# Performance work log

Hardware: AMD Instinct MI355X
Metric: run time of the kernel (lower is better)

The kernel has to match this reference:

```python
import jax, jax.numpy as jnp
import numpy as np

N, E = 16384, 262144
NS_N, NV_N = 128, 64      # node irreps: 128x0e + 64x1o
NS_E, NV_E = 64, 32       # edge irreps: 64x0e + 32x1o
C_OH, LAT = 16, 128
DS, DV = 128, 64          # irreps_out: 128x0e + 64x1o
GS = DS + DV              # gate input scalars (128 act scalars + 64 gates)
SC = 2 * NS_N + NS_E      # 320 concatenated scalar channels
VC = 2 * NV_N + NV_E      # 160 concatenated l=1 channels
M0_IN = SC + VC           # 480 m=0 features into SO2 linear
M0_OUT = GS + DV          # 256 m=0 outputs
AVG_NEI = 16.0
EPS = 1e-8


def setup_inputs() -> dict:
    key = jax.random.key(0)
    ks = jax.random.split(key, 20)
    f = lambda k, s: jax.random.normal(k, s, dtype=jnp.float32)
    return dict(
        node_feat=f(ks[0], (N, NS_N + 3 * NV_N)),
        edge_feat=f(ks[1], (E, NS_E + 3 * NV_E)),
        edge_vec=f(ks[2], (E, 3)),
        latents=f(ks[3], (E, LAT)),
        node_onehot=jax.nn.one_hot(jax.random.randint(ks[4], (N,), 0, C_OH), C_OH, dtype=jnp.float32),
        ln_n_g0=jnp.ones(NS_N), ln_n_b0=jnp.zeros(NS_N), ln_n_g1=jnp.ones(NV_N),
        ln_e_g0=jnp.ones(NS_E), ln_e_b0=jnp.zeros(NS_E), ln_e_g1=jnp.ones(NV_E),
        W_m0=f(ks[5], (M0_IN, M0_OUT)),
        w_r=f(ks[6], (VC, DV)), w_i=f(ks[7], (VC, DV)),
        W_env=f(ks[8], (LAT, DS + DV)),
        Wp0=f(ks[9], (DS, DS)), bp0=jnp.zeros(DS), Wpv=f(ks[10], (DV, DV)),
        Wtp0=f(ks[11], (DS, C_OH, GS)), Wtp1=f(ks[12], (DV, C_OH, DV)),
        Wo0=f(ks[13], (DS, DS)), bo0=jnp.zeros(DS), Wov=f(ks[14], (DV, DV)),
        res_param=jnp.zeros(()),
        edge_index=jax.random.randint(ks[15], (2, E), 0, N),
    )


def _sep_ln(s, v, g0, b0, g1):
    # separable equivariant layer norm: LN on scalars, per-sample RMS on l=1 block
    mu = s.mean(-1, keepdims=True)
    var = jnp.mean((s - mu) ** 2, -1, keepdims=True)
    s = (s - mu) * jax.lax.rsqrt(var + EPS) * g0 + b0
    vvar = jnp.mean(v * v, axis=(-2, -1), keepdims=True)  # component norm, degree-balanced (single l=1)
    v = v * jax.lax.rsqrt(vvar + EPS) * g1[None, :, None]
    return s, v


def _edge_frame(vec):
    # orthonormal frame (a, e1, e2) with a along the edge
    a = vec * jax.lax.rsqrt(jnp.sum(vec * vec, -1, keepdims=True) + EPS)
    helper = jnp.where(jnp.abs(a[:, 2:3]) < 0.99,
                       jnp.array([0.0, 0.0, 1.0], dtype=vec.dtype),
                       jnp.array([1.0, 0.0, 0.0], dtype=vec.dtype))
    e1 = jnp.cross(helper, a)
    e1 = e1 * jax.lax.rsqrt(jnp.sum(e1 * e1, -1, keepdims=True) + EPS)
    e2 = jnp.cross(a, e1)
    return a, e1, e2


def reference(node_feat, edge_feat, edge_vec, latents, node_onehot,
              ln_n_g0, ln_n_b0, ln_n_g1, ln_e_g0, ln_e_b0, ln_e_g1,
              W_m0, w_r, w_i, W_env, Wp0, bp0, Wpv,
              Wtp0, Wtp1, Wo0, bo0, Wov, res_param, edge_index):
    src, dst = edge_index[0], edge_index[1]
    ns, nv = node_feat[:, :NS_N], node_feat[:, NS_N:].reshape(-1, NV_N, 3)
    es, ev = edge_feat[:, :NS_E], edge_feat[:, NS_E:].reshape(-1, NV_E, 3)
    ns, nv = _sep_ln(ns, nv, ln_n_g0, ln_n_b0, ln_n_g1)
    es, ev = _sep_ln(es, ev, ln_e_g0, ln_e_b0, ln_e_g1)
    # per-edge concat: node[src] + edge + node[dst]
    s_cat = jnp.concatenate([ns[src], es, ns[dst]], -1)          # [E, SC]
    v_cat = jnp.concatenate([nv[src], ev, nv[dst]], 1)           # [E, VC, 3]
    # SO2 linear: rotate into edge frame, mix per |m|, rotate back
    a, e1, e2 = _edge_frame(edge_vec)
    c0 = jnp.einsum('eci,ei->ec', v_cat, a)
    c1 = jnp.einsum('eci,ei->ec', v_cat, e1)
    c2 = jnp.einsum('eci,ei->ec', v_cat, e2)
    m0 = jnp.concatenate([s_cat, c0], -1) @ W_m0 * (1.0 / np.sqrt(M0_IN))  # [E, M0_OUT]
    s_out, c0o = m0[:, :GS], m0[:, GS:]
    inv = 1.0 / np.sqrt(VC)
    c1o = (c1 @ w_r - c2 @ w_i) * inv
    c2o = (c1 @ w_i + c2 @ w_r) * inv
    v_out = (c0o[..., None] * a[:, None, :] + c1o[..., None] * e1[:, None, :]
             + c2o[..., None] * e2[:, None, :])                  # [E, DV, 3]
    # gate activation
    s_act = jax.nn.silu(s_out[:, :DS])
    gates = jax.nn.sigmoid(s_out[:, DS:])
    v_g = v_out * gates[..., None]
    # lin_post (per-l linear, scalar bias)
    s2 = s_act @ Wp0 * (1.0 / np.sqrt(DS)) + bp0
    v2 = jnp.einsum('eui,uv->evi', v_g, Wpv) * (1.0 / np.sqrt(DV))
    # env weighting from latents (E3ElementLinear, per-irrep-channel scalars)
    w = latents @ W_env * (1.0 / np.sqrt(LAT))
    s2 = s2 * w[:, :DS]
    v2 = v2 * w[:, DS:, None]
    nrm = 1.0 / np.sqrt(AVG_NEI)
    sa = jax.ops.segment_sum(s2, dst, num_segments=N) * nrm
    va = jax.ops.segment_sum(v2, dst, num_segments=N) * nrm
    # one-hot FullyConnectedTensorProduct (in2 all 0e) + gate + linear
    t0 = jnp.einsum('nu,nc,ucv->nv', sa, node_onehot, Wtp0) * (1.0 / np.sqrt(DS * C_OH))
    t1 = jnp.einsum('nui,nc,ucv->nvi', va, node_onehot, Wtp1) * (1.0 / np.sqrt(DV * C_OH))
    s3 = jax.nn.silu(t0[:, :DS])
    v3 = t1 * jax.nn.sigmoid(t0[:, DS:])[..., None]
    s4 = s3 @ Wo0 * (1.0 / np.sqrt(DS)) + bo0
    v4 = jnp.einsum('nui,uv->nvi', v3, Wov) * (1.0 / np.sqrt(DV))
    new = jnp.concatenate([s4, v4.reshape(-1, 3 * DV)], -1)
    r = jax.nn.sigmoid(res_param)
    return r * node_feat + (1.0 - r) * new
```

## Files before the change

kernel.cpp:

```cpp
#include <hip/hip_runtime.h>
#include <math.h>

#define N_NODES 16384
#define N_EDGES 262144
#define EPSF 1e-8f

#define OFF_XE    0
#define OFF_C12   14848
#define OFF_FR    35840
#define OFF_EDST  36608
#define OFF_ESRC  36736
#define POOL_BYTES 36864
#define OFF_SACT  0
#define OFF_GATE  8704
#define OFF_C0O   13312
#define OFF_C1O   17920
#define OFF_C2O   22528
#define OFF_VG    8704

typedef __bf16 bf16x8 __attribute__((ext_vector_type(8)));
typedef float  f32x4  __attribute__((ext_vector_type(4)));

__device__ __forceinline__ f32x4 MFMA16(bf16x8 a, bf16x8 b, f32x4 c){
  return __builtin_amdgcn_mfma_f32_16x16x32_bf16(a, b, c, 0, 0, 0);
// ... 87 lines not shown
}

__global__ __launch_bounds__(256) void k_node_ln(
    const float* __restrict__ nf, const float* __restrict__ g0,
    const float* __restrict__ b0, const float* __restrict__ g1,
    unsigned short* __restrict__ ns_ln, _Float16* __restrict__ nv_ln)
{
  const int tid  = threadIdx.x;
  const int lane = tid & 63;
  const int n    = blockIdx.x*4 + (tid>>6);
  const float* row = nf + (size_t)n*320;

  float s0 = row[lane], s1 = row[64+lane];
  float mu = wsum64(s0+s1) * (1.0f/128.0f);
  float d0 = s0-mu, d1 = s1-mu;
  float var = wsum64(d0*d0+d1*d1) * (1.0f/128.0f);
  float rs = rsqrtf(var + EPSF);
  ns_ln[(size_t)n*128 + lane]    = f2bf(d0*rs*g0[lane]    + b0[lane]);
  ns_ln[(size_t)n*128 + 64+lane] = f2bf(d1*rs*g0[64+lane] + b0[64+lane]);

  float px = row[128+lane*3+0], py = row[128+lane*3+1], pz = row[128+lane*3+2];
  float vvar = wsum64(px*px+py*py+pz*pz) * (1.0f/192.0f);
  float vsc = rsqrtf(vvar + EPSF) * g1[lane];
  nv_ln[(size_t)n*192 + lane*3+0] = (_Float16)(px*vsc);
  nv_ln[(size_t)n*192 + lane*3+1] = (_Float16)(py*vsc);
  nv_ln[(size_t)n*192 + lane*3+2] = (_Float16)(pz*vsc);
}

__global__ __launch_bounds__(256,4) void k_edge(
  const float* __restrict__ ef, const float* __restrict__ evec,
  const float* __restrict__ lats,
  const float* __restrict__ g0e, const float* __restrict__ b0e, const float* __restrict__ g1e,
  const unsigned short* __restrict__ pWm0, const unsigned short* __restrict__ pWc,
  const unsigned short* __restrict__ pWenv, const unsigned short* __restrict__ pWp0,
  const unsigned short* __restrict__ pWpv,
  const float* __restrict__ bp0,
  const int* __restrict__ eidx, const int* __restrict__ perm,
  const unsigned short* __restrict__ ns_ln, const _Float16* __restrict__ nv_ln,
  float* __restrict__ sa, float* __restrict__ va)
{
  extern __shared__ unsigned char pool[];
  const int tid = threadIdx.x;
  unsigned short* XE   = (unsigned short*)(pool + OFF_XE);
  unsigned short* C12s = (unsigned short*)(pool + OFF_C12);
  _Float16* FRh = (_Float16*)(pool + OFF_FR);
  int* EDST = (int*)(pool + OFF_EDST);
  int* ESRC = (int*)(pool + OFF_ESRC);

  const int nwg = gridDim.x;
  const int bswz = (blockIdx.x & 7)*(nwg>>3) + (blockIdx.x >> 3);

  const int wid = tid>>6, l = tid&63;
  const int r15 = l&15, g = l>>4;
  const int sbase = bswz*32;

  {
    const int ln = tid & 31;
    int psrc[4], pdst[4];
    float pvx[4], pvy[4], pvz[4];
    float pef0[4], pef1[4], pwx[4], pwy[4], pwz[4];
    #pragma unroll
    for (int eo=0; eo<4; ++eo){
      const int slot = sbase + eo*8 + (tid>>5);
      const int e = perm[slot];
      psrc[eo] = eidx[e];
      pdst[eo] = eidx[N_EDGES + e];
      pvx[eo] = evec[(size_t)e*3+0];
      pvy[eo] = evec[(size_t)e*3+1];
      pvz[eo] = evec[(size_t)e*3+2];
      const float* erow = ef + (size_t)e*160;
      pef0[eo] = erow[ln];
      pef1[eo] = erow[32+ln];
      pwx[eo]  = erow[64+ln*3+0];
      pwy[eo]  = erow[64+ln*3+1];
      pwz[eo]  = erow[64+ln*3+2];
    }
    _Float16 pns[4][6], pnd[4][6];
    #pragma unroll
    for (int eo=0; eo<4; ++eo){
      const _Float16* nvs = nv_ln + (size_t)psrc[eo]*192 + 3*ln;
      const _Float16* nvd = nv_ln + (size_t)pdst[eo]*192 + 3*ln;
      pns[eo][0]=nvs[0];  pns[eo][1]=nvs[1];  pns[eo][2]=nvs[2];
      pns[eo][3]=nvs[96]; pns[eo][4]=nvs[97]; pns[eo][5]=nvs[98];
      pnd[eo][0]=nvd[0];  pnd[eo][1]=nvd[1];  pnd[eo][2]=nvd[2];
      pnd[eo][3]=nvd[96]; pnd[eo][4]=nvd[97]; pnd[eo][5]=nvd[98];
    }

    #pragma unroll
    for (int eo=0; eo<4; ++eo){
      const int el = eo*8 + (tid>>5);
      const int src = psrc[eo];
      const int dst = pdst[eo];

      float vx=pvx[eo], vy=pvy[eo], vz=pvz[eo];
      float rn = rsqrtf(vx*vx+vy*vy+vz*vz+EPSF);
      float ax=vx*rn, ay=vy*rn, az=vz*rn;
      float hx, hz;
      if (fabsf(az) < 0.99f){ hx=0.f; hz=1.f; } else { hx=1.f; hz=0.f; }
      float e1x = -hz*ay;
      float e1y = hz*ax - hx*az;
      float e1z = hx*ay;
      float rn1 = rsqrtf(e1x*e1x+e1y*e1y+e1z*e1z+EPSF);
      e1x*=rn1; e1y*=rn1; e1z*=rn1;
      float e2x = ay*e1z - az*e1y;
      float e2y = az*e1x - ax*e1z;
      float e2z = ax*e1y - ay*e1x;
      if (ln==0){
        FRh[el*12+0]=(_Float16)ax;  FRh[el*12+1]=(_Float16)ay;  FRh[el*12+2]=(_Float16)az;
        FRh[el*12+3]=(_Float16)e1x; FRh[el*12+4]=(_Float16)e1y; FRh[el*12+5]=(_Float16)e1z;
        FRh[el*12+6]=(_Float16)e2x; FRh[el*12+7]=(_Float16)e2y; FRh[el*12+8]=(_Float16)e2z;
        EDST[el]=dst;
        ESRC[el]=src;
      }

      float s0=pef0[eo], s1=pef1[eo];
      float mu = wsum32(s0+s1)*(1.f/64.f);
      float d0=s0-mu, d1=s1-mu;
      float var = wsum32(d0*d0+d1*d1)*(1.f/64.f);
      float rs = rsqrtf(var+EPSF);
      XE[el*232 + ln]    = f2bf(d0*rs*g0e[ln]    + b0e[ln]);
      XE[el*232 + 32+ln] = f2bf(d1*rs*g0e[32+ln] + b0e[32+ln]);

      float wx=pwx[eo], wy=pwy[eo], wz=pwz[eo];
      float vvar = wsum32(wx*wx+wy*wy+wz*wz)*(1.f/96.f);
      float vsc = rsqrtf(vvar+EPSF)*g1e[ln];
      wx*=vsc; wy*=vsc; wz*=vsc;
      XE  [el*232 + 64+64+ln]    = f2bf(wx*ax +wy*ay +wz*az);
      C12s[el*328 + 64+ln]       = f2bf(wx*e1x+wy*e1y+wz*e1z);
      C12s[el*328 + 160+64+ln]   = f2bf(wx*e2x+wy*e2y+wz*e2z);

      #pragma unroll
      for (int q=0;q<2;q++){
        int u = ln+32*q;
        float px=(float)pns[eo][q*3+0], py=(float)pns[eo][q*3+1], pz=(float)pns[eo][q*3+2];
        XE  [el*232 + 64+u]      = f2bf(px*ax +py*ay +pz*az);
        C12s[el*328 + u]         = f2bf(px*e1x+py*e1y+pz*e1z);
        C12s[el*328 + 160+u]     = f2bf(px*e2x+py*e2y+pz*e2z);
        px=(float)pnd[eo][q*3+0]; py=(float)pnd[eo][q*3+1]; pz=(float)pnd[eo][q*3+2];
        XE  [el*232 + 64+96+u]   = f2bf(px*ax +py*ay +pz*az);
        C12s[el*328 + 96+u]      = f2bf(px*e1x+py*e1y+pz*e1z);
        C12s[el*328 + 160+96+u]  = f2bf(px*e2x+py*e2y+pz*e2z);
      }
    }
  }
  __syncthreads();

  const f32x4 zero4 = {0.f,0.f,0.f,0.f};

  f32x4 acc1[2][4];
  #pragma unroll
  for (int m=0;m<2;m++)
    #pragma unroll
    for (int n=0;n<4;n++) acc1[m][n]=zero4;
  {
    const unsigned short* bbase = pWm0 + ((size_t)(wid*64 + r15)*4 + g)*8;
    bf16x8 gA[2][8];
    {
      const int rs0 = ESRC[r15], rs1 = ESRC[16+r15];
      const int rd0 = EDST[r15], rd1 = EDST[16+r15];
      #pragma unroll
      for (int q=0;q<4;q++){
        gA[0][q]   = *(const bf16x8*)&ns_ln[(size_t)rs0*128 + q*32 + g*8];
        gA[1][q]   = *(const bf16x8*)&ns_ln[(size_t)rs1*128 + q*32 + g*8];
        gA[0][4+q] = *(const bf16x8*)&ns_ln[(size_t)rd0*128 + q*32 + g*8];
        gA[1][4+q] = *(const bf16x8*)&ns_ln[(size_t)rd1*128 + q*32 + g*8];
      }
    }
    #pragma unroll
    for (int t=0;t<7;t++){
      const int kc  = (t<2) ? (4+t) : (10 + t-2);
      const int col = (t<2) ? (t*32) : (64 + (t-2)*32);
      bf16x8 a0 = *(const bf16x8*)&XE[(    r15)*232 + col + g*8];
      bf16x8 a1 = *(const bf16x8*)&XE[(16+ r15)*232 + col + g*8];
      const unsigned short* bp = bbase + (size_t)kc*8192;
      #pragma unroll
      for (int n=0;n<4;n++){
        bf16x8 b = *(const bf16x8*)(bp + n*512);
        acc1[0][n] = MFMA16(a0,b,acc1[0][n]);
        acc1[1][n] = MFMA16(a1,b,acc1[1][n]);
      }
    }
    #pragma unroll
    for (int t=0;t<8;t++){
      const int kc = (t<4) ? t : (6 + t-4);
      const unsigned short* bp = bbase + (size_t)kc*8192;
      #pragma unroll
      for (int n=0;n<4;n++){
        bf16x8 b = *(const bf16x8*)(bp + n*512);
        acc1[0][n] = MFMA16(gA[0][t],b,acc1[0][n]);
        acc1[1][n] = MFMA16(gA[1][t],b,acc1[1][n]);
      }
    }
  }

  f32x4 acc2[2][2];
  #pragma unroll
  for (int m=0;m<2;m++){ acc2[m][0]=zero4; acc2[m][1]=zero4; }
  {
    const unsigned short* bbase = pWc + ((size_t)(wid*32 + r15)*4 + g)*8;
    #pragma unroll
    for (int kc=0;kc<10;kc++){
      bf16x8 a0 = *(const bf16x8*)&C12s[(    r15)*328 + kc*32 + g*8];
      bf16x8 a1 = *(const bf16x8*)&C12s[(16+ r15)*328 + kc*32 + g*8];
      const unsigned short* bp = bbase + (size_t)kc*4096;
      #pragma unroll
      for (int n=0;n<2;n++){
        bf16x8 b = *(const bf16x8*)(bp + n*512);
        acc2[0][n] = MFMA16(a0,b,acc2[0][n]);
        acc2[1][n] = MFMA16(a1,b,acc2[1][n]);
      }
    }
  }

  float wsc[2][2][4], wvc[2][4];
  {
    f32x4 acc3[2][3];
    #pragma unroll
    for (int m=0;m<2;m++)
      #pragma unroll
      for (int n=0;n<3;n++) acc3[m][n]=zero4;
    const int eg0 = perm[sbase + r15];
    const int eg1 = perm[sbase + 16 + r15];
    const float* la0 = lats + (size_t)eg0*128;
    const float* la1 = lats + (size_t)eg1*128;
    const int colb0 = wid*32, colb1 = wid*32+16, colb2 = 128+wid*16;
    #pragma unroll
    for (int kc=0;kc<4;kc++){
      float4 f00 = *(const float4*)&la0[kc*32 + g*8];
      float4 f01 = *(const float4*)&la0[kc*32 + g*8 + 4];
      float4 f10 = *(const float4*)&la1[kc*32 + g*8];
      float4 f11 = *(const float4*)&la1[kc*32 + g*8 + 4];
      union { bf16x8 v; unsigned short s[8]; } a0, a1;
      a0.s[0]=f2bf(f00.x); a0.s[1]=f2bf(f00.y); a0.s[2]=f2bf(f00.z); a0.s[3]=f2bf(f00.w);
      a0.s[4]=f2bf(f01.x); a0.s[5]=f2bf(f01.y); a0.s[6]=f2bf(f01.z); a0.s[7]=f2bf(f01.w);
      a1.s[0]=f2bf(f10.x); a1.s[1]=f2bf(f10.y); a1.s[2]=f2bf(f10.z); a1.s[3]=f2bf(f10.w);
      a1.s[4]=f2bf(f11.x); a1.s[5]=f2bf(f11.y); a1.s[6]=f2bf(f11.z); a1.s[7]=f2bf(f11.w);
      bf16x8 b0 = *(const bf16x8*)(pWenv + ((size_t)(kc*192 + colb0 + r15)*4 + g)*8);
      bf16x8 b1 = *(const bf16x8*)(pWenv + ((size_t)(kc*192 + colb1 + r15)*4 + g)*8);
      bf16x8 b2 = *(const bf16x8*)(pWenv + ((size_t)(kc*192 + colb2 + r15)*4 + g)*8);
      acc3[0][0] = MFMA16(a0.v,b0,acc3[0][0]);
      acc3[1][0] = MFMA16(a1.v,b0,acc3[1][0]);
      acc3[0][1] = MFMA16(a0.v,b1,acc3[0][1]);
      acc3[1][1] = MFMA16(a1.v,b1,acc3[1][1]);
      acc3[0][2] = MFMA16(a0.v,b2,acc3[0][2]);
      acc3[1][2] = MFMA16(a1.v,b2,acc3[1][2]);
    }
    const float S = 0.08838834764831845f;
    #pragma unroll
    for (int m=0;m<2;m++)
      #pragma unroll
      for (int r=0;r<4;r++){
        wsc[m][0][r] = acc3[m][0][r]*S;
        wsc[m][1][r] = acc3[m][1][r]*S;
        wvc[m][r]    = acc3[m][2][r]*S;
      }
  }

  float bp0v[2];
  #pragma unroll
  for (int n=0;n<2;n++) bp0v[n] = bp0[wid*32 + n*16 + r15];

  __syncthreads();

  {
    unsigned short* SAs = (unsigned short*)(pool + OFF_SACT);
    unsigned short* GAb = (unsigned short*)(pool + OFF_GATE);
    unsigned short* C0b = (unsigned short*)(pool + OFF_C0O);
    #pragma unroll
    for (int m=0;m<2;m++)
      #pragma unroll
      for (int n=0;n<4;n++)
        #pragma unroll
        for (int r=0;r<4;r++){
          int e = m*16 + g*4 + r;
          int j = wid*64 + n*16 + r15;
          float v = acc1[m][n][r]*0.04564354645876384f;
          if (j < 128)      SAs[e*136 + j] = f2bf(silu(v));
          else if (j < 192) GAb[e*72 + (j-128)] = f2bf(sigm(v));
          else              C0b[e*72 + (j-192)] = f2bf(v);
        }
    unsigned short* C1b = (unsigned short*)(pool + OFF_C1O);
    unsigned short* C2b = (unsigned short*)(pool + OFF_C2O);
    #pragma unroll
    for (int m=0;m<2;m++)
      #pragma unroll
      for (int n=0;n<2;n++)
        #pragma unroll
        for (int r=0;r<4;r++){
          int e = m*16 + g*4 + r;
          int j = wid*32 + n*16 + r15;
          float v = acc2[m][n][r]*0.07905694150420949f;
          if (j < 64) C1b[e*72 + j] = f2bf(v);
          else        C2b[e*72 + (j-64)] = f2bf(v);
        }
  }
  __syncthreads();

  {
    const int e = tid>>3, u0 = (tid&7)*8;
    const unsigned short* GAb = (const unsigned short*)(pool + OFF_GATE);
    const unsigned short* C0b = (const unsigned short*)(pool + OFF_C0O);
    const unsigned short* C1b = (const unsigned short*)(pool + OFF_C1O);
    const unsigned short* C2b = (const unsigned short*)(pool + OFF_C2O);
    float ax=(float)FRh[e*12+0],  ay=(float)FRh[e*12+1],  az=(float)FRh[e*12+2];
    float b1x=(float)FRh[e*12+3], b1y=(float)FRh[e*12+4], b1z=(float)FRh[e*12+5];
    float b2x=(float)FRh[e*12+6], b2y=(float)FRh[e*12+7], b2z=(float)FRh[e*12+8];
    float vgx[8], vgy[8], vgz[8];
    #pragma unroll
    for (int i=0;i<8;i++){
      int u = u0+i;
      float gt = bf2f(GAb[e*72+u]);
      float c0 = bf2f(C0b[e*72+u]), c1 = bf2f(C1b[e*72+u]), c2 = bf2f(C2b[e*72+u]);
      vgx[i] = (c0*ax + c1*b1x + c2*b2x)*gt;
      vgy[i] = (c0*ay + c1*b1y + c2*b2y)*gt;
      vgz[i] = (c0*az + c1*b1z + c2*b2z)*gt;
    }
    __syncthreads();
    unsigned short* VGs = (unsigned short*)(pool + OFF_VG);
    #pragma unroll
    for (int i=0;i<8;i++){
      VGs[0*2304 + e*72 + u0+i] = f2bf(vgx[i]);
      VGs[1*2304 + e*72 + u0+i] = f2bf(vgy[i]);
      VGs[2*2304 + e*72 + u0+i] = f2bf(vgz[i]);
    }
  }
  __syncthreads();

  {
    const unsigned short* SAs = (const unsigned short*)(pool + OFF_SACT);
    const unsigned short* VGs = (const unsigned short*)(pool + OFF_VG);

    f32x4 acc4[2][2], acc5[3][2];
    #pragma unroll
    for (int m=0;m<2;m++){ acc4[m][0]=zero4; acc4[m][1]=zero4; }
    #pragma unroll
    for (int c=0;c<3;c++){ acc5[c][0]=zero4; acc5[c][1]=zero4; }

    {
      const unsigned short* bbase = pWp0 + ((size_t)(wid*32 + r15)*4 + g)*8;
      #pragma unroll
      for (int kc=0;kc<4;kc++){
        bf16x8 a0 = *(const bf16x8*)&SAs[(    r15)*136 + kc*32 + g*8];
        bf16x8 a1 = *(const bf16x8*)&SAs[(16+ r15)*136 + kc*32 + g*8];
        #pragma unroll
        for (int n=0;n<2;n++){
          bf16x8 b = *(const bf16x8*)(bbase + (size_t)kc*4096 + n*512);
          acc4[0][n] = MFMA16(a0,b,acc4[0][n]);
          acc4[1][n] = MFMA16(a1,b,acc4[1][n]);
        }
      }
    }
    {
      bf16x8 b5[2];
      #pragma unroll
      for (int kc=0;kc<2;kc++)
        b5[kc] = *(const bf16x8*)(pWpv + ((size_t)(kc*64 + wid*16 + r15)*4 + g)*8);
      #pragma unroll
      for (int c=0;c<3;c++)
        #pragma unroll
        for (int kc=0;kc<2;kc++){
          bf16x8 a0 = *(const bf16x8*)&VGs[c*2304 + (    r15)*72 + kc*32 + g*8];
          bf16x8 a1 = *(const bf16x8*)&VGs[c*2304 + (16+ r15)*72 + kc*32 + g*8];
          acc5[c][0] = MFMA16(a0,b5[kc],acc5[c][0]);
          acc5[c][1] = MFMA16(a1,b5[kc],acc5[c][1]);
        }
    }

    __syncthreads();
    _Float16* R = (_Float16*)pool;
    #pragma unroll
    for (int m=0;m<2;m++)
      #pragma unroll
      for (int n=0;n<2;n++)
        #pragma unroll
        for (int r=0;r<4;r++){
          int e = m*16 + g*4 + r;
          int j = wid*32 + n*16 + r15;
          R[e*320 + j] = (_Float16)((acc4[m][n][r]*0.08838834764831845f + bp0v[n]) * wsc[m][n][r]);
        }
    #pragma unroll
    for (int c=0;c<3;c++)
      #pragma unroll
      for (int m=0;m<2;m++)
        #pragma unroll
        for (int r=0;r<4;r++){
          int e = m*16 + g*4 + r;
          int vch = wid*16 + r15;
          R[e*320 + 128 + vch*3 + c] = (_Float16)(acc5[c][m][r]*0.125f * wvc[m][r]);
        }
    __syncthreads();

    for (int j = tid; j < 320; j += 256){
      float accv = (float)R[j];
      int cur = EDST[0];
      for (int e=1;e<32;e++){
        int d = EDST[e];
        float v = (float)R[e*320 + j];
        if (d != cur){
          float* tgt = (j<128) ? &sa[(size_t)cur*128 + j] : &va[(size_t)cur*192 + (j-128)];
          atomicAdd(tgt, accv);
          accv = v; cur = d;
        } else accv += v;
      }
      float* tgt = (j<128) ? &sa[(size_t)cur*128 + j] : &va[(size_t)cur*192 + (j-128)];
      atomicAdd(tgt, accv);
    }
  }
}

__global__ __launch_bounds__(256) void k_node_out(
  const float* __restrict__ nf, const float* __restrict__ oh,
  const float* __restrict__ Wtp0, const float* __restrict__ Wtp1,
  const float* __restrict__ Wo0, const float* __restrict__ bo0,
  const float* __restrict__ Wov, const float* __restrict__ resp,
  const float* __restrict__ sa, const float* __restrict__ va,
  float* __restrict__ out)
{
  __shared__ float SAB[4][128];
  __shared__ float VX[4][64], VY[4][64], VZ[4][64];
  __shared__ float S3 [4][128];
  __shared__ float V3 [4][256];
  const int tid=threadIdx.x, lane=tid&63, g=tid>>6;
  const int n = blockIdx.x*4 + g;

  float cf=0.f;
  #pragma unroll
  for (int j=0;j<16;j++) cf += j*oh[(size_t)n*16+j];
  const int c = (int)(cf+0.5f);

  SAB[g][lane]    = sa[(size_t)n*128+lane]   *0.25f;
  SAB[g][64+lane] = sa[(size_t)n*128+64+lane]*0.25f;
  VX[g][lane] = va[(size_t)n*192+lane*3+0]*0.25f;
  VY[g][lane] = va[(size_t)n*192+lane*3+1]*0.25f;
  VZ[g][lane] = va[(size_t)n*192+lane*3+2]*0.25f;
  __syncthreads();

  float t00=0.f, t01=0.f, t02=0.f;
  const float* w0c = Wtp0 + (size_t)c*192;
  for (int u=0;u<128;u++){
    float s = SAB[g][u];
    t00 += s * w0c[(size_t)u*3072 + lane];
    t01 += s * w0c[(size_t)u*3072 + lane+64];
    t02 += s * w0c[(size_t)u*3072 + lane+128];
  }
  const float sct0 = 0.02209708691f;
  t00*=sct0; t01*=sct0; t02*=sct0;

  float t1x=0.f,t1y=0.f,t1z=0.f;
  const float* w1c = Wtp1 + (size_t)c*64;
  for (int u=0;u<64;u++){
    float wv = w1c[(size_t)u*1024 + lane];
    t1x += VX[g][u]*wv;
    t1y += VY[g][u]*wv;
    t1z += VZ[g][u]*wv;
  }
  t1x*=0.03125f; t1y*=0.03125f; t1z*=0.03125f;

  S3[g][lane]    = silu(t00);
// ... 37 lines not shown
  const float* nf   = (const float*)d_in[0];
  const float* ef   = (const float*)d_in[1];
  const float* evec = (const float*)d_in[2];
  const float* lats = (const float*)d_in[3];
  const float* oh   = (const float*)d_in[4];
  const float* g0n  = (const float*)d_in[5];
  const float* b0n  = (const float*)d_in[6];
  const float* g1n  = (const float*)d_in[7];
  const float* g0e  = (const float*)d_in[8];
  const float* b0e  = (const float*)d_in[9];
  const float* g1e  = (const float*)d_in[10];
  const float* Wm0  = (const float*)d_in[11];
  const float* wr   = (const float*)d_in[12];
  const float* wi   = (const float*)d_in[13];
  const float* Wenv = (const float*)d_in[14];
  const float* Wp0  = (const float*)d_in[15];
  const float* bp0  = (const float*)d_in[16];
  const float* Wpv  = (const float*)d_in[17];
  const float* Wtp0 = (const float*)d_in[18];
  const float* Wtp1 = (const float*)d_in[19];
  const float* Wo0  = (const float*)d_in[20];
  const float* bo0  = (const float*)d_in[21];
  const float* Wov  = (const float*)d_in[22];
  const float* resp = (const float*)d_in[23];
  const int*   eidx = (const int*)d_in[24];

  char* base = (char*)d_ws;
  unsigned short* ns_ln = (unsigned short*)(base);
  _Float16* nv_ln = (_Float16*)(base + 4194304);
  float* sa    = (float*)(base + 10485760);
  float* va    = (float*)(base + 18874368);
  unsigned short* wpk = (unsigned short*)(base + 31457280);
  unsigned short* pWm0  = wpk;
  unsigned short* pWc   = wpk + 122880;
  unsigned short* pWenv = wpk + 163840;
  unsigned short* pWp0  = wpk + 188416;
  unsigned short* pWpv  = wpk + 204800;
  int* ibuf   = (int*)(base + 31875072);
  int* cnt    = ibuf;
  int* rowp   = ibuf + 16384;
  int* cursor = ibuf + 32769;
  int* perm   = ibuf + 49153;

  hipMemsetAsync(sa, 0, (size_t)N_NODES*320*sizeof(float), stream);
  hipMemsetAsync(cnt, 0, N_NODES*sizeof(int), stream);

  k_pack_all<<<(208896+255)/256, 256, 0, stream>>>(Wm0, wr, wi, Wenv, Wp0, Wpv, wpk);
  k_node_ln<<<N_NODES/4, 256, 0, stream>>>(nf, g0n, b0n, g1n, ns_ln, nv_ln);

  k_hist<<<(N_EDGES+255)/256, 256, 0, stream>>>(eidx, cnt);
  k_scan<<<1, 256, 0, stream>>>(cnt, rowp, cursor);
  k_fill<<<(N_EDGES+255)/256, 256, 0, stream>>>(eidx, cursor, perm);

  k_edge<<<N_EDGES/32, 256, POOL_BYTES, stream>>>(ef, evec, lats, g0e, b0e, g1e,
                                                  pWm0, pWc, pWenv, pWp0, pWpv, bp0,
                                                  eidx, perm, ns_ln, nv_ln,
                                                  sa, va);
  k_node_out<<<N_NODES/4, 256, 0, stream>>>(nf, oh, Wtp0, Wtp1, Wo0, bo0, Wov,
                                            resp, sa, va, (float*)d_out);
}
```

Measured before the change: 558.5 us.

## Process two 32-edge tiles per edge block and prefetch next tile's indices

The edge kernel now handles 64 edges per workgroup in two sequential 32-edge tiles, halving the grid. During the first tile it prefetches the permutation index, src/dst and edge vector for the second tile, so those dependent gather latencies overlap with the first tile's compute. The cost is fewer workgroups in flight, extra registers held across the loop, and an added barrier per tile.

```diff
diff --git a/kernel.cpp b/kernel.cpp
--- a/kernel.cpp
+++ b/kernel.cpp
@@ -163,358 +163,386 @@
 
   const int wid = tid>>6, l = tid&63;
   const int r15 = l&15, g = l>>4;
-  const int sbase = bswz*32;
-
+  const int ln = tid & 31;
+
+  int psrc[4], pdst[4];
+  float pvx[4], pvy[4], pvz[4];
+  int pei[4];
   {
-    const int ln = tid & 31;
-    int psrc[4], pdst[4];
-    float pvx[4], pvy[4], pvz[4];
-    float pef0[4], pef1[4], pwx[4], pwy[4], pwz[4];
+    const int sb0 = bswz*64;
     #pragma unroll
     for (int eo=0; eo<4; ++eo){
-      const int slot = sbase + eo*8 + (tid>>5);
+      const int slot = sb0 + eo*8 + (tid>>5);
       const int e = perm[slot];
+      pei[eo] = e;
       psrc[eo] = eidx[e];
       pdst[eo] = eidx[N_EDGES + e];
       pvx[eo] = evec[(size_t)e*3+0];
       pvy[eo] = evec[(size_t)e*3+1];
       pvz[eo] = evec[(size_t)e*3+2];
-      const float* erow = ef + (size_t)e*160;
-      pef0[eo] = erow[ln];
-      pef1[eo] = erow[32+ln];
-      pwx[eo]  = erow[64+ln*3+0];
-      pwy[eo]  = erow[64+ln*3+1];
-      pwz[eo]  = erow[64+ln*3+2];
-    }
-    _Float16 pns[4][6], pnd[4][6];
-    #pragma unroll
-    for (int eo=0; eo<4; ++eo){
-      const _Float16* nvs = nv_ln + (size_t)psrc[eo]*192 + 3*ln;
-      const _Float16* nvd = nv_ln + (size_t)pdst[eo]*192 + 3*ln;
-      pns[eo][0]=nvs[0];  pns[eo][1]=nvs[1];  pns[eo][2]=nvs[2];
-      pns[eo][3]=nvs[96]; pns[eo][4]=nvs[97]; pns[eo][5]=nvs[98];
-      pnd[eo][0]=nvd[0];  pnd[eo][1]=nvd[1];  pnd[eo][2]=nvd[2];
-      pnd[eo][3]=nvd[96]; pnd[eo][4]=nvd[97]; pnd[eo][5]=nvd[98];
-    }
-
-    #pragma unroll
-    for (int eo=0; eo<4; ++eo){
-      const int el = eo*8 + (tid>>5);
-      const int src = psrc[eo];
-      const int dst = pdst[eo];
-
-      float vx=pvx[eo], vy=pvy[eo], vz=pvz[eo];
-      float rn = rsqrtf(vx*vx+vy*vy+vz*vz+EPSF);
-      float ax=vx*rn, ay=vy*rn, az=vz*rn;
-      float hx, hz;
-      if (fabsf(az) < 0.99f){ hx=0.f; hz=1.f; } else { hx=1.f; hz=0.f; }
-      float e1x = -hz*ay;
-      float e1y = hz*ax - hx*az;
-      float e1z = hx*ay;
-      float rn1 = rsqrtf(e1x*e1x+e1y*e1y+e1z*e1z+EPSF);
-      e1x*=rn1; e1y*=rn1; e1z*=rn1;
-      float e2x = ay*e1z - az*e1y;
-      float e2y = az*e1x - ax*e1z;
-      float e2z = ax*e1y - ay*e1x;
-      if (ln==0){
-        FRh[el*12+0]=(_Float16)ax;  FRh[el*12+1]=(_Float16)ay;  FRh[el*12+2]=(_Float16)az;
-        FRh[el*12+3]=(_Float16)e1x; FRh[el*12+4]=(_Float16)e1y; FRh[el*12+5]=(_Float16)e1z;
-        FRh[el*12+6]=(_Float16)e2x; FRh[el*12+7]=(_Float16)e2y; FRh[el*12+8]=(_Float16)e2z;
-        EDST[el]=dst;
-        ESRC[el]=src;
-      }
-
-      float s0=pef0[eo], s1=pef1[eo];
-      float mu = wsum32(s0+s1)*(1.f/64.f);
-      float d0=s0-mu, d1=s1-mu;
-      float var = wsum32(d0*d0+d1*d1)*(1.f/64.f);
-      float rs = rsqrtf(var+EPSF);
-      XE[el*232 + ln]    = f2bf(d0*rs*g0e[ln]    + b0e[ln]);
-      XE[el*232 + 32+ln] = f2bf(d1*rs*g0e[32+ln] + b0e[32+ln]);
-
-      float wx=pwx[eo], wy=pwy[eo], wz=pwz[eo];
-      float vvar = wsum32(wx*wx+wy*wy+wz*wz)*(1.f/96.f);
-      float vsc = rsqrtf(vvar+EPSF)*g1e[ln];
-      wx*=vsc; wy*=vsc; wz*=vsc;
-      XE  [el*232 + 64+64+ln]    = f2bf(wx*ax +wy*ay +wz*az);
-      C12s[el*328 + 64+ln]       = f2bf(wx*e1x+wy*e1y+wz*e1z);
-      C12s[el*328 + 160+64+ln]   = f2bf(wx*e2x+wy*e2y+wz*e2z);
-
-      #pragma unroll
-      for (int q=0;q<2;q++){
-        int u = ln+32*q;
-        float px=(float)pns[eo][q*3+0], py=(float)pns[eo][q*3+1], pz=(float)pns[eo][q*3+2];
-        XE  [el*232 + 64+u]      = f2bf(px*ax +py*ay +pz*az);
-        C12s[el*328 + u]         = f2bf(px*e1x+py*e1y+pz*e1z);
-        C12s[el*328 + 160+u]     = f2bf(px*e2x+py*e2y+pz*e2z);
-        px=(float)pnd[eo][q*3+0]; py=(float)pnd[eo][q*3+1]; pz=(float)pnd[eo][q*3+2];
-        XE  [el*232 + 64+96+u]   = f2bf(px*ax +py*ay +pz*az);
-        C12s[el*328 + 96+u]      = f2bf(px*e1x+py*e1y+pz*e1z);
-        C12s[el*328 + 160+96+u]  = f2bf(px*e2x+py*e2y+pz*e2z);
-      }
-    }
-  }
-  __syncthreads();
-
-  const f32x4 zero4 = {0.f,0.f,0.f,0.f};
-
-  f32x4 acc1[2][4];
-  #pragma unroll
-  for (int m=0;m<2;m++)
-    #pragma unroll
-    for (int n=0;n<4;n++) acc1[m][n]=zero4;
-  {
-    const unsigned short* bbase = pWm0 + ((size_t)(wid*64 + r15)*4 + g)*8;
-    bf16x8 gA[2][8];
+    }
+  }
+
+  for (int tt=0; tt<2; ++tt){
+    const int sbase = bswz*64 + tt*32;
+    __syncthreads();
+
     {
-      const int rs0 = ESRC[r15], rs1 = ESRC[16+r15];
-      const int rd0 = EDST[r15], rd1 = EDST[16+r15];
-      #pragma unroll
-      for (int q=0;q<4;q++){
-        gA[0][q]   = *(const bf16x8*)&ns_ln[(size_t)rs0*128 + q*32 + g*8];
-        gA[1][q]   = *(const bf16x8*)&ns_ln[(size_t)rs1*128 + q*32 + g*8];
-        gA[0][4+q] = *(const bf16x8*)&ns_ln[(size_t)rd0*128 + q*32 + g*8];
-        gA[1][4+q] = *(const bf16x8*)&ns_ln[(size_t)rd1*128 + q*32 + g*8];
-      }
-    }
-    #pragma unroll
-    for (int t=0;t<7;t++){
-      const int kc  = (t<2) ? (4+t) : (10 + t-2);
-      const int col = (t<2) ? (t*32) : (64 + (t-2)*32);
-      bf16x8 a0 = *(const bf16x8*)&XE[(    r15)*232 + col + g*8];
-      bf16x8 a1 = *(const bf16x8*)&XE[(16+ r15)*232 + col + g*8];
-      const unsigned short* bp = bbase + (size_t)kc*8192;
-      #pragma unroll
-      for (int n=0;n<4;n++){
-        bf16x8 b = *(const bf16x8*)(bp + n*512);
-        acc1[0][n] = MFMA16(a0,b,acc1[0][n]);
-        acc1[1][n] = MFMA16(a1,b,acc1[1][n]);
-      }
-    }
-    #pragma unroll
-    for (int t=0;t<8;t++){
-      const int kc = (t<4) ? t : (6 + t-4);
-      const unsigned short* bp = bbase + (size_t)kc*8192;
-      #pragma unroll
-      for (int n=0;n<4;n++){
-        bf16x8 b = *(const bf16x8*)(bp + n*512);
-        acc1[0][n] = MFMA16(gA[0][t],b,acc1[0][n]);
-        acc1[1][n] = MFMA16(gA[1][t],b,acc1[1][n]);
-      }
-    }
-  }
-
-  f32x4 acc2[2][2];
-  #pragma unroll
-  for (int m=0;m<2;m++){ acc2[m][0]=zero4; acc2[m][1]=zero4; }
-  {
-    const unsigned short* bbase = pWc + ((size_t)(wid*32 + r15)*4 + g)*8;
-    #pragma unroll
-    for (int kc=0;kc<10;kc++){
-      bf16x8 a0 = *(const bf16x8*)&C12s[(    r15)*328 + kc*32 + g*8];
-      bf16x8 a1 = *(const bf16x8*)&C12s[(16+ r15)*328 + kc*32 + g*8];
-      const unsigned short* bp = bbase + (size_t)kc*4096;
-      #pragma unroll
-      for (int n=0;n<2;n++){
-        bf16x8 b = *(const bf16x8*)(bp + n*512);
-        acc2[0][n] = MFMA16(a0,b,acc2[0][n]);
-        acc2[1][n] = MFMA16(a1,b,acc2[1][n]);
-      }
-    }
-  }
-
-  float wsc[2][2][4], wvc[2][4];
-  {
-    f32x4 acc3[2][3];
+      float pef0[4], pef1[4], pwx[4], pwy[4], pwz[4];
+      #pragma unroll
+      for (int eo=0; eo<4; ++eo){
+        const float* erow = ef + (size_t)pei[eo]*160;
+        pef0[eo] = erow[ln];
+        pef1[eo] = erow[32+ln];
+        pwx[eo]  = erow[64+ln*3+0];
+        pwy[eo]  = erow[64+ln*3+1];
+        pwz[eo]  = erow[64+ln*3+2];
+      }
+      _Float16 pns[4][6], pnd[4][6];
+      #pragma unroll
+      for (int eo=0; eo<4; ++eo){
+        const _Float16* nvs = nv_ln + (size_t)psrc[eo]*192 + 3*ln;
+        const _Float16* nvd = nv_ln + (size_t)pdst[eo]*192 + 3*ln;
+        pns[eo][0]=nvs[0];  pns[eo][1]=nvs[1];  pns[eo][2]=nvs[2];
+        pns[eo][3]=nvs[96]; pns[eo][4]=nvs[97]; pns[eo][5]=nvs[98];
+        pnd[eo][0]=nvd[0];  pnd[eo][1]=nvd[1];  pnd[eo][2]=nvd[2];
+        pnd[eo][3]=nvd[96]; pnd[eo][4]=nvd[97]; pnd[eo][5]=nvd[98];
+      }
+
+      #pragma unroll
+      for (int eo=0; eo<4; ++eo){
+        const int el = eo*8 + (tid>>5);
+        const int src = psrc[eo];
+        const int dst = pdst[eo];
+
+        float vx=pvx[eo], vy=pvy[eo], vz=pvz[eo];
+        float rn = rsqrtf(vx*vx+vy*vy+vz*vz+EPSF);
+        float ax=vx*rn, ay=vy*rn, az=vz*rn;
+        float hx, hz;
+        if (fabsf(az) < 0.99f){ hx=0.f; hz=1.f; } else { hx=1.f; hz=0.f; }
+        float e1x = -hz*ay;
+        float e1y = hz*ax - hx*az;
+        float e1z = hx*ay;
+        float rn1 = rsqrtf(e1x*e1x+e1y*e1y+e1z*e1z+EPSF);
+        e1x*=rn1; e1y*=rn1; e1z*=rn1;
+        float e2x = ay*e1z - az*e1y;
+        float e2y = az*e1x - ax*e1z;
+        float e2z = ax*e1y - ay*e1x;
+        if (ln==0){
+          FRh[el*12+0]=(_Float16)ax;  FRh[el*12+1]=(_Float16)ay;  FRh[el*12+2]=(_Float16)az;
+          FRh[el*12+3]=(_Float16)e1x; FRh[el*12+4]=(_Float16)e1y; FRh[el*12+5]=(_Float16)e1z;
+          FRh[el*12+6]=(_Float16)e2x; FRh[el*12+7]=(_Float16)e2y; FRh[el*12+8]=(_Float16)e2z;
+          EDST[el]=dst;
+          ESRC[el]=src;
+        }
+
+        float s0=pef0[eo], s1=pef1[eo];
+        float mu = wsum32(s0+s1)*(1.f/64.f);
+        float d0=s0-mu, d1=s1-mu;
+        float var = wsum32(d0*d0+d1*d1)*(1.f/64.f);
+        float rs = rsqrtf(var+EPSF);
+        XE[el*232 + ln]    = f2bf(d0*rs*g0e[ln]    + b0e[ln]);
+        XE[el*232 + 32+ln] = f2bf(d1*rs*g0e[32+ln] + b0e[32+ln]);
+
+        float wx=pwx[eo], wy=pwy[eo], wz=pwz[eo];
+        float vvar = wsum32(wx*wx+wy*wy+wz*wz)*(1.f/96.f);
+        float vsc = rsqrtf(vvar+EPSF)*g1e[ln];
+        wx*=vsc; wy*=vsc; wz*=vsc;
+        XE  [el*232 + 64+64+ln]    = f2bf(wx*ax +wy*ay +wz*az);
+        C12s[el*328 + 64+ln]       = f2bf(wx*e1x+wy*e1y+wz*e1z);
+        C12s[el*328 + 160+64+ln]   = f2bf(wx*e2x+wy*e2y+wz*e2z);
+
+        #pragma unroll
+        for (int q=0;q<2;q++){
+          int u = ln+32*q;
+          float px=(float)pns[eo][q*3+0], py=(float)pns[eo][q*3+1], pz=(float)pns[eo][q*3+2];
+          XE  [el*232 + 64+u]      = f2bf(px*ax +py*ay +pz*az);
+          C12s[el*328 + u]         = f2bf(px*e1x+py*e1y+pz*e1z);
+          C12s[el*328 + 160+u]     = f2bf(px*e2x+py*e2y+pz*e2z);
+          px=(float)pnd[eo][q*3+0]; py=(float)pnd[eo][q*3+1]; pz=(float)pnd[eo][q*3+2];
+          XE  [el*232 + 64+96+u]   = f2bf(px*ax +py*ay +pz*az);
+          C12s[el*328 + 96+u]      = f2bf(px*e1x+py*e1y+pz*e1z);
+          C12s[el*328 + 160+96+u]  = f2bf(px*e2x+py*e2y+pz*e2z);
+        }
+      }
+    }
+
+    if (tt==0){
+      const int sb1 = bswz*64 + 32;
+      #pragma unroll
+      for (int eo=0; eo<4; ++eo){
+        const int slot = sb1 + eo*8 + (tid>>5);
+        const int e = perm[slot];
+        pei[eo] = e;
+        psrc[eo] = eidx[e];
+        pdst[eo] = eidx[N_EDGES + e];
+        pvx[eo] = evec[(size_t)e*3+0];
+        pvy[eo] = evec[(size_t)e*3+1];
+        pvz[eo] = evec[(size_t)e*3+2];
+      }
+    }
+    __syncthreads();
+
+    const f32x4 zero4 = {0.f,0.f,0.f,0.f};
+
+    f32x4 acc1[2][4];
     #pragma unroll
     for (int m=0;m<2;m++)
       #pragma unroll
-      for (int n=0;n<3;n++) acc3[m][n]=zero4;
-    const int eg0 = perm[sbase + r15];
-    const int eg1 = perm[sbase + 16 + r15];
-    const float* la0 = lats + (size_t)eg0*128;
-    const float* la1 = lats + (size_t)eg1*128;
-    const int colb0 = wid*32, colb1 = wid*32+16, colb2 = 128+wid*16;
+      for (int n=0;n<4;n++) acc1[m][n]=zero4;
+    {
+      const unsigned short* bbase = pWm0 + ((size_t)(wid*64 + r15)*4 + g)*8;
+      bf16x8 gA[2][8];
+      {
+        const int rs0 = ESRC[r15], rs1 = ESRC[16+r15];
+        const int rd0 = EDST[r15], rd1 = EDST[16+r15];
+        #pragma unroll
+        for (int q=0;q<4;q++){
+          gA[0][q]   = *(const bf16x8*)&ns_ln[(size_t)rs0*128 + q*32 + g*8];
+          gA[1][q]   = *(const bf16x8*)&ns_ln[(size_t)rs1*128 + q*32 + g*8];
+          gA[0][4+q] = *(const bf16x8*)&ns_ln[(size_t)rd0*128 + q*32 + g*8];
+          gA[1][4+q] = *(const bf16x8*)&ns_ln[(size_t)rd1*128 + q*32 + g*8];
+        }
+      }
+      #pragma unroll
+      for (int t=0;t<7;t++){
+        const int kc  = (t<2) ? (4+t) : (10 + t-2);
+        const int col = (t<2) ? (t*32) : (64 + (t-2)*32);
+        bf16x8 a0 = *(const bf16x8*)&XE[(    r15)*232 + col + g*8];
+        bf16x8 a1 = *(const bf16x8*)&XE[(16+ r15)*232 + col + g*8];
+        const unsigned short* bp = bbase + (size_t)kc*8192;
+        #pragma unroll
+        for (int n=0;n<4;n++){
+          bf16x8 b = *(const bf16x8*)(bp + n*512);
+          acc1[0][n] = MFMA16(a0,b,acc1[0][n]);
+          acc1[1][n] = MFMA16(a1,b,acc1[1][n]);
+        }
+      }
+      #pragma unroll
+      for (int t=0;t<8;t++){
+        const int kc = (t<4) ? t : (6 + t-4);
+        const unsigned short* bp = bbase + (size_t)kc*8192;
+        #pragma unroll
+        for (int n=0;n<4;n++){
+          bf16x8 b = *(const bf16x8*)(bp + n*512);
+          acc1[0][n] = MFMA16(gA[0][t],b,acc1[0][n]);
+          acc1[1][n] = MFMA16(gA[1][t],b,acc1[1][n]);
+        }
+      }
+    }
+
+    f32x4 acc2[2][2];
     #pragma unroll
-    for (int kc=0;kc<4;kc++){
-      float4 f00 = *(const float4*)&la0[kc*32 + g*8];
-      float4 f01 = *(const float4*)&la0[kc*32 + g*8 + 4];
-      float4 f10 = *(const float4*)&la1[kc*32 + g*8];
-      float4 f11 = *(const float4*)&la1[kc*32 + g*8 + 4];
-      union { bf16x8 v; unsigned short s[8]; } a0, a1;
-      a0.s[0]=f2bf(f00.x); a0.s[1]=f2bf(f00.y); a0.s[2]=f2bf(f00.z); a0.s[3]=f2bf(f00.w);
-      a0.s[4]=f2bf(f01.x); a0.s[5]=f2bf(f01.y); a0.s[6]=f2bf(f01.z); a0.s[7]=f2bf(f01.w);
-      a1.s[0]=f2bf(f10.x); a1.s[1]=f2bf(f10.y); a1.s[2]=f2bf(f10.z); a1.s[3]=f2bf(f10.w);
-      a1.s[4]=f2bf(f11.x); a1.s[5]=f2bf(f11.y); a1.s[6]=f2bf(f11.z); a1.s[7]=f2bf(f11.w);
-      bf16x8 b0 = *(const bf16x8*)(pWenv + ((size_t)(kc*192 + colb0 + r15)*4 + g)*8);
-      bf16x8 b1 = *(const bf16x8*)(pWenv + ((size_t)(kc*192 + colb1 + r15)*4 + g)*8);
-      bf16x8 b2 = *(const bf16x8*)(pWenv + ((size_t)(kc*192 + colb2 + r15)*4 + g)*8);
-      acc3[0][0] = MFMA16(a0.v,b0,acc3[0][0]);
-      acc3[1][0] = MFMA16(a1.v,b0,acc3[1][0]);
-      acc3[0][1] = MFMA16(a0.v,b1,acc3[0][1]);
-      acc3[1][1] = MFMA16(a1.v,b1,acc3[1][1]);
-      acc3[0][2] = MFMA16(a0.v,b2,acc3[0][2]);
-      acc3[1][2] = MFMA16(a1.v,b2,acc3[1][2]);
-    }
-    const float S = 0.08838834764831845f;
+    for (int m=0;m<2;m++){ acc2[m][0]=zero4; acc2[m][1]=zero4; }
+    {
+      const unsigned short* bbase = pWc + ((size_t)(wid*32 + r15)*4 + g)*8;
+      #pragma unroll
+      for (int kc=0;kc<10;kc++){
+        bf16x8 a0 = *(const bf16x8*)&C12s[(    r15)*328 + kc*32 + g*8];
+        bf16x8 a1 = *(const bf16x8*)&C12s[(16+ r15)*328 + kc*32 + g*8];
+        const unsigned short* bp = bbase + (size_t)kc*4096;
+        #pragma unroll
+        for (int n=0;n<2;n++){
+          bf16x8 b = *(const bf16x8*)(bp + n*512);
+          acc2[0][n] = MFMA16(a0,b,acc2[0][n]);
+          acc2[1][n] = MFMA16(a1,b,acc2[1][n]);
+        }
+      }
+    }
+
+    float wsc[2][2][4], wvc[2][4];
+    {
+      f32x4 acc3[2][3];
+      #pragma unroll
+      for (int m=0;m<2;m++)
+        #pragma unroll
+        for (int n=0;n<3;n++) acc3[m][n]=zero4;
+      const int eg0 = perm[sbase + r15];
+      const int eg1 = perm[sbase + 16 + r15];
+      const float* la0 = lats + (size_t)eg0*128;
+      const float* la1 = lats + (size_t)eg1*128;
+      const int colb0 = wid*32, colb1 = wid*32+16, colb2 = 128+wid*16;
+      #pragma unroll
+      for (int kc=0;kc<4;kc++){
+        float4 f00 = *(const float4*)&la0[kc*32 + g*8];
+        float4 f01 = *(const float4*)&la0[kc*32 + g*8 + 4];
+        float4 f10 = *(const float4*)&la1[kc*32 + g*8];
+        float4 f11 = *(const float4*)&la1[kc*32 + g*8 + 4];
+        union { bf16x8 v; unsigned short s[8]; } a0, a1;
+        a0.s[0]=f2bf(f00.x); a0.s[1]=f2bf(f00.y); a0.s[2]=f2bf(f00.z); a0.s[3]=f2bf(f00.w);
+        a0.s[4]=f2bf(f01.x); a0.s[5]=f2bf(f01.y); a0.s[6]=f2bf(f01.z); a0.s[7]=f2bf(f01.w);
+        a1.s[0]=f2bf(f10.x); a1.s[1]=f2bf(f10.y); a1.s[2]=f2bf(f10.z); a1.s[3]=f2bf(f10.w);
+        a1.s[4]=f2bf(f11.x); a1.s[5]=f2bf(f11.y); a1.s[6]=f2bf(f11.z); a1.s[7]=f2bf(f11.w);
+        bf16x8 b0 = *(const bf16x8*)(pWenv + ((size_t)(kc*192 + colb0 + r15)*4 + g)*8);
+        bf16x8 b1 = *(const bf16x8*)(pWenv + ((size_t)(kc*192 + colb1 + r15)*4 + g)*8);
+        bf16x8 b2 = *(const bf16x8*)(pWenv + ((size_t)(kc*192 + colb2 + r15)*4 + g)*8);
+        acc3[0][0] = MFMA16(a0.v,b0,acc3[0][0]);
+        acc3[1][0] = MFMA16(a1.v,b0,acc3[1][0]);
+        acc3[0][1] = MFMA16(a0.v,b1,acc3[0][1]);
+        acc3[1][1] = MFMA16(a1.v,b1,acc3[1][1]);
+        acc3[0][2] = MFMA16(a0.v,b2,acc3[0][2]);
+        acc3[1][2] = MFMA16(a1.v,b2,acc3[1][2]);
+      }
+      const float S = 0.08838834764831845f;
+      #pragma unroll
+      for (int m=0;m<2;m++)
+        #pragma unroll
+        for (int r=0;r<4;r++){
+          wsc[m][0][r] = acc3[m][0][r]*S;
+          wsc[m][1][r] = acc3[m][1][r]*S;
+          wvc[m][r]    = acc3[m][2][r]*S;
+        }
+    }
+
+    float bp0v[2];
     #pragma unroll
-    for (int m=0;m<2;m++)
-      #pragma unroll
-      for (int r=0;r<4;r++){
-        wsc[m][0][r] = acc3[m][0][r]*S;
-        wsc[m][1][r] = acc3[m][1][r]*S;
-        wvc[m][r]    = acc3[m][2][r]*S;
-      }
-  }
-
-  float bp0v[2];
-  #pragma unroll
-  for (int n=0;n<2;n++) bp0v[n] = bp0[wid*32 + n*16 + r15];
-
-  __syncthreads();
-
-  {
-    unsigned short* SAs = (unsigned short*)(pool + OFF_SACT);
-    unsigned short* GAb = (unsigned short*)(pool + OFF_GATE);
-    unsigned short* C0b = (unsigned short*)(pool + OFF_C0O);
-    #pragma unroll
-    for (int m=0;m<2;m++)
-      #pragma unroll
-      for (int n=0;n<4;n++)
-        #pragma unroll
-        for (int r=0;r<4;r++){
-          int e = m*16 + g*4 + r;
-          int j = wid*64 + n*16 + r15;
-          float v = acc1[m][n][r]*0.04564354645876384f;
-          if (j < 128)      SAs[e*136 + j] = f2bf(silu(v));
-          else if (j < 192) GAb[e*72 + (j-128)] = f2bf(sigm(v));
-          else              C0b[e*72 + (j-192)] = f2bf(v);
-        }
-    unsigned short* C1b = (unsigned short*)(pool + OFF_C1O);
-    unsigned short* C2b = (unsigned short*)(pool + OFF_C2O);
-    #pragma unroll
-    for (int m=0;m<2;m++)
-      #pragma unroll
-      for (int n=0;n<2;n++)
-        #pragma unroll
-        for (int r=0;r<4;r++){
-          int e = m*16 + g*4 + r;
-          int j = wid*32 + n*16 + r15;
-          float v = acc2[m][n][r]*0.07905694150420949f;
-          if (j < 64) C1b[e*72 + j] = f2bf(v);
-          else        C2b[e*72 + (j-64)] = f2bf(v);
-        }
-  }
-  __syncthreads();
-
-  {
-    const int e = tid>>3, u0 = (tid&7)*8;
-    const unsigned short* GAb = (const unsigned short*)(pool + OFF_GATE);
-    const unsigned short* C0b = (const unsigned short*)(pool + OFF_C0O);
-    const unsigned short* C1b = (const unsigned short*)(pool + OFF_C1O);
-    const unsigned short* C2b = (const unsigned short*)(pool + OFF_C2O);
-    float ax=(float)FRh[e*12+0],  ay=(float)FRh[e*12+1],  az=(float)FRh[e*12+2];
-    float b1x=(float)FRh[e*12+3], b1y=(float)FRh[e*12+4], b1z=(float)FRh[e*12+5];
-    float b2x=(float)FRh[e*12+6], b2y=(float)FRh[e*12+7], b2z=(float)FRh[e*12+8];
-    float vgx[8], vgy[8], vgz[8];
-    #pragma unroll
-    for (int i=0;i<8;i++){
-      int u = u0+i;
-      float gt = bf2f(GAb[e*72+u]);
-      float c0 = bf2f(C0b[e*72+u]), c1 = bf2f(C1b[e*72+u]), c2 = bf2f(C2b[e*72+u]);
-      vgx[i] = (c0*ax + c1*b1x + c2*b2x)*gt;
-      vgy[i] = (c0*ay + c1*b1y + c2*b2y)*gt;
-      vgz[i] = (c0*az + c1*b1z + c2*b2z)*gt;
-    }
+    for (int n=0;n<2;n++) bp0v[n] = bp0[wid*32 + n*16 + r15];
+
     __syncthreads();
-    unsigned short* VGs = (unsigned short*)(pool + OFF_VG);
-    #pragma unroll
-    for (int i=0;i<8;i++){
-      VGs[0*2304 + e*72 + u0+i] = f2bf(vgx[i]);
-      VGs[1*2304 + e*72 + u0+i] = f2bf(vgy[i]);
-      VGs[2*2304 + e*72 + u0+i] = f2bf(vgz[i]);
-    }
-  }
-  __syncthreads();
-
-  {
-    const unsigned short* SAs = (const unsigned short*)(pool + OFF_SACT);
-    const unsigned short* VGs = (const unsigned short*)(pool + OFF_VG);
-
-    f32x4 acc4[2][2], acc5[3][2];
-    #pragma unroll
-    for (int m=0;m<2;m++){ acc4[m][0]=zero4; acc4[m][1]=zero4; }
-    #pragma unroll
-    for (int c=0;c<3;c++){ acc5[c][0]=zero4; acc5[c][1]=zero4; }
 
     {
-      const unsigned short* bbase = pWp0 + ((size_t)(wid*32 + r15)*4 + g)*8;
-      #pragma unroll
-      for (int kc=0;kc<4;kc++){
-        bf16x8 a0 = *(const bf16x8*)&SAs[(    r15)*136 + kc*32 + g*8];
-        bf16x8 a1 = *(const bf16x8*)&SAs[(16+ r15)*136 + kc*32 + g*8];
-        #pragma unroll
-        for (int n=0;n<2;n++){
-          bf16x8 b = *(const bf16x8*)(bbase + (size_t)kc*4096 + n*512);
-          acc4[0][n] = MFMA16(a0,b,acc4[0][n]);
-          acc4[1][n] = MFMA16(a1,b,acc4[1][n]);
-        }
-      }
-    }
+      unsigned short* SAs = (unsigned short*)(pool + OFF_SACT);
+      unsigned short* GAb = (unsigned short*)(pool + OFF_GATE);
+      unsigned short* C0b = (unsigned short*)(pool + OFF_C0O);
+      #pragma unroll
+      for (int m=0;m<2;m++)
+        #pragma unroll
+        for (int n=0;n<4;n++)
+          #pragma unroll
+          for (int r=0;r<4;r++){
+            int e = m*16 + g*4 + r;
+            int j = wid*64 + n*16 + r15;
+            float v = acc1[m][n][r]*0.04564354645876384f;
+            if (j < 128)      SAs[e*136 + j] = f2bf(silu(v));
+            else if (j < 192) GAb[e*72 + (j-128)] = f2bf(sigm(v));
+            else              C0b[e*72 + (j-192)] = f2bf(v);
+          }
+      unsigned short* C1b = (unsigned short*)(pool + OFF_C1O);
+      unsigned short* C2b = (unsigned short*)(pool + OFF_C2O);
+      #pragma unroll
+      for (int m=0;m<2;m++)
+        #pragma unroll
+        for (int n=0;n<2;n++)
+          #pragma unroll
+          for (int r=0;r<4;r++){
+            int e = m*16 + g*4 + r;
+            int j = wid*32 + n*16 + r15;
+            float v = acc2[m][n][r]*0.07905694150420949f;
+            if (j < 64) C1b[e*72 + j] = f2bf(v);
+            else        C2b[e*72 + (j-64)] = f2bf(v);
+          }
+    }
+    __syncthreads();
+
     {
-      bf16x8 b5[2];
-      #pragma unroll
-      for (int kc=0;kc<2;kc++)
-        b5[kc] = *(const bf16x8*)(pWpv + ((size_t)(kc*64 + wid*16 + r15)*4 + g)*8);
+      const int e = tid>>3, u0 = (tid&7)*8;
+      const unsigned short* GAb = (const unsigned short*)(pool + OFF_GATE);
+      const unsigned short* C0b = (const unsigned short*)(pool + OFF_C0O);
+      const unsigned short* C1b = (const unsigned short*)(pool + OFF_C1O);
+      const unsigned short* C2b = (const unsigned short*)(pool + OFF_C2O);
+      float ax=(float)FRh[e*12+0],  ay=(float)FRh[e*12+1],  az=(float)FRh[e*12+2];
+      float b1x=(float)FRh[e*12+3], b1y=(float)FRh[e*12+4], b1z=(float)FRh[e*12+5];
+      float b2x=(float)FRh[e*12+6], b2y=(float)FRh[e*12+7], b2z=(float)FRh[e*12+8];
+      float vgx[8], vgy[8], vgz[8];
+      #pragma unroll
+      for (int i=0;i<8;i++){
+        int u = u0+i;
+        float gt = bf2f(GAb[e*72+u]);
+        float c0 = bf2f(C0b[e*72+u]), c1 = bf2f(C1b[e*72+u]), c2 = bf2f(C2b[e*72+u]);
+        vgx[i] = (c0*ax + c1*b1x + c2*b2x)*gt;
+        vgy[i] = (c0*ay + c1*b1y + c2*b2y)*gt;
+        vgz[i] = (c0*az + c1*b1z + c2*b2z)*gt;
+      }
+      __syncthreads();
+      unsigned short* VGs = (unsigned short*)(pool + OFF_VG);
+      #pragma unroll
+      for (int i=0;i<8;i++){
+        VGs[0*2304 + e*72 + u0+i] = f2bf(vgx[i]);
+        VGs[1*2304 + e*72 + u0+i] = f2bf(vgy[i]);
+        VGs[2*2304 + e*72 + u0+i] = f2bf(vgz[i]);
+      }
+    }
+    __syncthreads();
+
+    {
+      const unsigned short* SAs = (const unsigned short*)(pool + OFF_SACT);
+      const unsigned short* VGs = (const unsigned short*)(pool + OFF_VG);
+
+      f32x4 acc4[2][2], acc5[3][2];
+      #pragma unroll
+      for (int m=0;m<2;m++){ acc4[m][0]=zero4; acc4[m][1]=zero4; }
+      #pragma unroll
+      for (int c=0;c<3;c++){ acc5[c][0]=zero4; acc5[c][1]=zero4; }
+
+      {
+        const unsigned short* bbase = pWp0 + ((size_t)(wid*32 + r15)*4 + g)*8;
+        #pragma unroll
+        for (int kc=0;kc<4;kc++){
+          bf16x8 a0 = *(const bf16x8*)&SAs[(    r15)*136 + kc*32 + g*8];
+          bf16x8 a1 = *(const bf16x8*)&SAs[(16+ r15)*136 + kc*32 + g*8];
+          #pragma unroll
+          for (int n=0;n<2;n++){
+            bf16x8 b = *(const bf16x8*)(bbase + (size_t)kc*4096 + n*512);
+            acc4[0][n] = MFMA16(a0,b,acc4[0][n]);
+            acc4[1][n] = MFMA16(a1,b,acc4[1][n]);
+          }
+        }
+      }
+      {
+        bf16x8 b5[2];
+        #pragma unroll
+        for (int kc=0;kc<2;kc++)
+          b5[kc] = *(const bf16x8*)(pWpv + ((size_t)(kc*64 + wid*16 + r15)*4 + g)*8);
+        #pragma unroll
+        for (int c=0;c<3;c++)
+          #pragma unroll
+          for (int kc=0;kc<2;kc++){
+            bf16x8 a0 = *(const bf16x8*)&VGs[c*2304 + (    r15)*72 + kc*32 + g*8];
+            bf16x8 a1 = *(const bf16x8*)&VGs[c*2304 + (16+ r15)*72 + kc*32 + g*8];
+            acc5[c][0] = MFMA16(a0,b5[kc],acc5[c][0]);
+            acc5[c][1] = MFMA16(a1,b5[kc],acc5[c][1]);
+          }
+      }
+
+      __syncthreads();
+      _Float16* R = (_Float16*)pool;
+      #pragma unroll
+      for (int m=0;m<2;m++)
+        #pragma unroll
+        for (int n=0;n<2;n++)
+          #pragma unroll
+          for (int r=0;r<4;r++){
+            int e = m*16 + g*4 + r;
+            int j = wid*32 + n*16 + r15;
+            R[e*320 + j] = (_Float16)((acc4[m][n][r]*0.08838834764831845f + bp0v[n]) * wsc[m][n][r]);
+          }
       #pragma unroll
       for (int c=0;c<3;c++)
         #pragma unroll
-        for (int kc=0;kc<2;kc++){
-          bf16x8 a0 = *(const bf16x8*)&VGs[c*2304 + (    r15)*72 + kc*32 + g*8];
-          bf16x8 a1 = *(const bf16x8*)&VGs[c*2304 + (16+ r15)*72 + kc*32 + g*8];
-          acc5[c][0] = MFMA16(a0,b5[kc],acc5[c][0]);
-          acc5[c][1] = MFMA16(a1,b5[kc],acc5[c][1]);
-        }
-    }
-
-    __syncthreads();
-    _Float16* R = (_Float16*)pool;
-    #pragma unroll
-    for (int m=0;m<2;m++)
-      #pragma unroll
-      for (int n=0;n<2;n++)
-        #pragma unroll
-        for (int r=0;r<4;r++){
-          int e = m*16 + g*4 + r;
-          int j = wid*32 + n*16 + r15;
-          R[e*320 + j] = (_Float16)((acc4[m][n][r]*0.08838834764831845f + bp0v[n]) * wsc[m][n][r]);
-        }
-    #pragma unroll
-    for (int c=0;c<3;c++)
-      #pragma unroll
-      for (int m=0;m<2;m++)
-        #pragma unroll
-        for (int r=0;r<4;r++){
-          int e = m*16 + g*4 + r;
-          int vch = wid*16 + r15;
-          R[e*320 + 128 + vch*3 + c] = (_Float16)(acc5[c][m][r]*0.125f * wvc[m][r]);
-        }
-    __syncthreads();
-
-    for (int j = tid; j < 320; j += 256){
-      float accv = (float)R[j];
-      int cur = EDST[0];
-      for (int e=1;e<32;e++){
-        int d = EDST[e];
-        float v = (float)R[e*320 + j];
-        if (d != cur){
-          float* tgt = (j<128) ? &sa[(size_t)cur*128 + j] : &va[(size_t)cur*192 + (j-128)];
-          atomicAdd(tgt, accv);
-          accv = v; cur = d;
-        } else accv += v;
-      }
-      float* tgt = (j<128) ? &sa[(size_t)cur*128 + j] : &va[(size_t)cur*192 + (j-128)];
-      atomicAdd(tgt, accv);
+        for (int m=0;m<2;m++)
+          #pragma unroll
+          for (int r=0;r<4;r++){
+            int e = m*16 + g*4 + r;
+            int vch = wid*16 + r15;
+            R[e*320 + 128 + vch*3 + c] = (_Float16)(acc5[c][m][r]*0.125f * wvc[m][r]);
+          }
+      __syncthreads();
+
+      for (int j = tid; j < 320; j += 256){
+        float accv = (float)R[j];
+        int cur = EDST[0];
+        for (int e=1;e<32;e++){
+          int d = EDST[e];
+          float v = (float)R[e*320 + j];
+          if (d != cur){
+            float* tgt = (j<128) ? &sa[(size_t)cur*128 + j] : &va[(size_t)cur*192 + (j-128)];
+            atomicAdd(tgt, accv);
+            accv = v; cur = d;
+          } else accv += v;
+        }
+        float* tgt = (j<128) ? &sa[(size_t)cur*128 + j] : &va[(size_t)cur*192 + (j-128)];
+        atomicAdd(tgt, accv);
+      }
     }
   }
 }
@@ -658,7 +686,7 @@
   k_scan<<<1, 256, 0, stream>>>(cnt, rowp, cursor);
   k_fill<<<(N_EDGES+255)/256, 256, 0, stream>>>(eidx, cursor, perm);
 
-  k_edge<<<N_EDGES/32, 256, POOL_BYTES, stream>>>(ef, evec, lats, g0e, b0e, g1e,
+  k_edge<<<N_EDGES/64, 256, POOL_BYTES, stream>>>(ef, evec, lats, g0e, b0e, g1e,
                                                   pWm0, pWc, pWenv, pWp0, pWpv, bp0,
                                                   eidx, perm, ns_ln, nv_ln,
                                                   sa, va);
```

Result: slower. 1.969 ms (+252.5%).
